# Kernel optimization log

Measured on AMD Instinct MI355X. Metric: run time of the kernel, lower is better.

The kernel has to match this reference:

```python
import jax, jax.numpy as jnp
import numpy as np

EMBED_DIM = 1024
NUM_HEADS = 16
HEAD_DIM = EMBED_DIM // NUM_HEADS


def setup_inputs() -> dict:
    key = jax.random.key(0)
    ks = jax.random.split(key, 5)
    s = 0.02
    return {
        "x": jax.random.normal(ks[0], (2, 2048, EMBED_DIM), dtype=jnp.float32),
        "w_qkv": jax.random.normal(ks[1], (EMBED_DIM, 3 * EMBED_DIM), dtype=jnp.float32) * s,
        "b_qkv": jnp.zeros((3 * EMBED_DIM,), dtype=jnp.float32),
        "w_out": jax.random.normal(ks[2], (EMBED_DIM, EMBED_DIM), dtype=jnp.float32) * s,
        "b_out": jnp.zeros((EMBED_DIM,), dtype=jnp.float32),
    }


def reference(x, w_qkv, b_qkv, w_out, b_out):
    B, T, C = x.shape
    qkv = x @ w_qkv + b_qkv                       # [B,T,3C]
    q, k, v = jnp.split(qkv, 3, axis=-1)
    # [B,T,C] -> [B,H,T,Dh]
    def heads(t):
        return t.reshape(B, T, NUM_HEADS, HEAD_DIM).transpose(0, 2, 1, 3)
    q, k, v = heads(q), heads(k), heads(v)
    scale = 1.0 / np.sqrt(HEAD_DIM).astype(np.float32)
    scores = jnp.einsum("bhqd,bhkd->bhqk", q, k) * scale  # [B,H,T,T]
    causal = jnp.tril(jnp.ones((T, T), dtype=bool))
    scores = jnp.where(causal[None, None], scores, -jnp.inf)
    attn = jax.nn.softmax(scores, axis=-1)
    out = jnp.einsum("bhqk,bhkd->bhqd", attn, v)  # [B,H,T,Dh]
    out = out.transpose(0, 2, 1, 3).reshape(B, T, C)
    return out @ w_out + b_out
```

## Files before the change

kernel.cpp:

```cpp
#include <hip/hip_runtime.h>

typedef unsigned short u16;
typedef unsigned int u32;
typedef __attribute__((ext_vector_type(2))) unsigned int u32x2;
typedef __attribute__((ext_vector_type(8))) short bf16x8;
typedef __attribute__((ext_vector_type(4))) float f32x4;
typedef __attribute__((ext_vector_type(16))) float f32x16;

#define TOK   4096
#define EMB   1024
#define NQKV  3072
#define TSEQ  2048
#define NH    16

__device__ __forceinline__ u16 f2b(float f) {
  union { float f; unsigned u; } v; v.f = f;
  unsigned r = v.u + 0x7FFFu + ((v.u >> 16) & 1u);
  return (u16)(r >> 16);
}

__device__ __forceinline__ u16 f2b_hu(float f) {
  return (u16)((__float_as_uint(f) + 0x8000u) >> 16);
}

__device__ __forceinline__ u32 pack_rn(float a, float b) {
  u32 ua = __float_as_uint(a) + 0x8000u;
  u32 ub = __float_as_uint(b) + 0x8000u;
  return __builtin_amdgcn_perm(ub, ua, 0x07060302u);
}

__device__ __forceinline__ f32x16 zero16() {
  f32x16 z;
#pragma unroll
  for (int i = 0; i < 16; i++) z[i] = 0.f;
  return z;
}

__device__ __forceinline__ void gload16(const void* g, void* l) {
  __builtin_amdgcn_global_load_lds((const __attribute__((address_space(1))) void*)g,
                                   (__attribute__((address_space(3))) void*)l, 16, 0, 0);
}


__global__ __launch_bounds__(256) void prep_kernel(const float* __restrict__ x,
                                                   u16* __restrict__ x_bf,
                                                   const float* __restrict__ w_qkv,
                                                   u16* __restrict__ wqkvT,
                                                   const float* __restrict__ w_out,
                                                   u16* __restrict__ woutT) {
  __shared__ u16 sm[64][65];
  int bid = blockIdx.x, tid = threadIdx.x;
  if (bid < 4096) {
    int i = bid * 256 + tid;
    float4 v = ((const float4*)x)[i];
    union { u16 us[4]; uint2 u2; } o;
    o.us[0] = f2b(v.x); o.us[1] = f2b(v.y); o.us[2] = f2b(v.z); o.us[3] = f2b(v.w);
    ((uint2*)x_bf)[i] = o.u2;
    return;
  }
  const float* src; u16* dst; int R, C, bx, by;
  if (bid < 4096 + 768) {
    int t = bid - 4096; bx = t % 48; by = t / 48;
    src = w_qkv; dst = wqkvT; R = EMB; C = NQKV;
  } else {
    int t = bid - 4096 - 768; bx = t & 15; by = t >> 4;
    src = w_out; dst = woutT; R = EMB; C = EMB;
  }
  int c0 = bx * 64, r0 = by * 64;
#pragma unroll
  for (int i = 0; i < 16; i++) {
    int idx = tid + i * 256;
    int r = idx >> 6, c = idx & 63;
    sm[r][c] = f2b(src[(size_t)(r0 + r) * C + c0 + c]);
  }
  __syncthreads();
  int cc2 = tid >> 2, rr0 = (tid & 3) * 16;
  union { u16 us[16]; uint4 v4[2]; } o;
#pragma unroll
  for (int j = 0; j < 16; j++) o.us[j] = sm[rr0 + j][cc2];
  *(uint4*)&dst[(size_t)(c0 + cc2) * R + r0 + rr0]     = o.v4[0];
  *(uint4*)&dst[(size_t)(c0 + cc2) * R + r0 + rr0 + 8] = o.v4[1];
}


template <int MODE, int TN>
__global__ __launch_bounds__(256) void gemm_bt(const u16* __restrict__ A,
                                               const u16* __restrict__ Bt,
                                               const float* __restrict__ bias,
                                               u16* __restrict__ qb, u16* __restrict__ kb,
                                               u16* __restrict__ vb, float* __restrict__ outp,
                                               int K, int N) {
  constexpr int CT = TN / 32;
  constexpr int RB = TN / 32;
  __shared__ u16 As[2][128][64];
  __shared__ u16 Bs[2][TN][64];
  int tid = threadIdx.x;
  int m0 = blockIdx.y * 128, n0 = blockIdx.x * TN;
  int lane = tid & 63, wid = tid >> 6;
  int wm = (wid >> 1) * 64;
  int wn = (wid & 1) * (TN / 2);
  int l15 = lane & 15, quad = lane >> 4;
  int srow = lane >> 3;
  int scol = (((lane & 7) ^ srow) * 8);

  f32x4 acc[4][CT];
#pragma unroll
  for (int i = 0; i < 4; i++)
#pragma unroll
    for (int j = 0; j < CT; j++) acc[i][j] = (f32x4){0.f, 0.f, 0.f, 0.f};

  const u16* Ag = A + (size_t)(m0 + wid * 32 + srow) * K + scol;
  const u16* Bg = Bt + (size_t)(n0 + wid * (TN / 4) + srow) * K + scol;

#pragma unroll
  for (int i = 0; i < 4; i++)
    gload16(Ag + (size_t)(i * 8) * K, &As[0][wid * 32 + i * 8][0]);
#pragma unroll
  for (int i = 0; i < RB; i++)
    gload16(Bg + (size_t)(i * 8) * K, &Bs[0][wid * (TN / 4) + i * 8][0]);
  __syncthreads();

  int cur = 0;
  for (int k0 = 0; k0 < K; k0 += 64) {
    if (k0 + 64 < K) {
      int kn = k0 + 64;
#pragma unroll
      for (int i = 0; i < 4; i++)
        gload16(Ag + (size_t)(i * 8) * K + kn, &As[cur ^ 1][wid * 32 + i * 8][0]);
#pragma unroll
      for (int i = 0; i < RB; i++)
        gload16(Bg + (size_t)(i * 8) * K + kn, &Bs[cur ^ 1][wid * (TN / 4) + i * 8][0]);
    }

#pragma unroll
    for (int ks = 0; ks < 2; ks++) {
      bf16x8 af[4], bfr[CT];
#pragma unroll
      for (int rt = 0; rt < 4; rt++)
        af[rt] = *(const bf16x8*)&As[cur][wm + rt * 16 + l15][((ks * 4 + quad) ^ (l15 & 7)) * 8];
#pragma unroll
      for (int ct = 0; ct < CT; ct++)
        bfr[ct] = *(const bf16x8*)&Bs[cur][wn + ct * 16 + l15][((ks * 4 + quad) ^ (l15 & 7)) * 8];
#pragma unroll
      for (int rt = 0; rt < 4; rt++)
#pragma unroll
        for (int ct = 0; ct < CT; ct++)
          acc[rt][ct] = __builtin_amdgcn_mfma_f32_16x16x32_bf16(bfr[ct], af[rt], acc[rt][ct], 0, 0, 0);
    }
    __syncthreads();
    cur ^= 1;
  }

#pragma unroll
  for (int rt = 0; rt < 4; rt++) {
#pragma unroll
    for (int ct = 0; ct < CT; ct++) {
      int m = m0 + wm + rt * 16 + l15;
      int nb = n0 + wn + ct * 16 + quad * 4;
      float4 b4 = *(const float4*)&bias[nb];
      float v0 = acc[rt][ct][0] + b4.x, v1 = acc[rt][ct][1] + b4.y;
      float v2 = acc[rt][ct][2] + b4.z, v3 = acc[rt][ct][3] + b4.w;
      if (MODE == 0) {
        int sel = nb >> 10;
        int c = nb & 1023;
        int h = c >> 6, d0 = c & 63;
        int b = m >> 11, t = m & 2047;
        if (sel == 2) {
          size_t vbase = ((((size_t)b * NH + h) * 64 + d0) * TSEQ) + t;
          vb[vbase]            = f2b_hu(v0);
          vb[vbase + TSEQ]     = f2b_hu(v1);
          vb[vbase + 2 * TSEQ] = f2b_hu(v2);
          vb[vbase + 3 * TSEQ] = f2b_hu(v3);
        } else {
          u16* dst = sel ? kb : qb;
          union { u32 u[2]; uint2 u2; } o;
          o.u[0] = pack_rn(v0, v1);
          o.u[1] = pack_rn(v2, v3);
          *(uint2*)&dst[((((size_t)b * NH + h) * TSEQ + t) << 6) + d0] = o.u2;
        }
      } else {
        float4 o = {v0, v1, v2, v3};
        *(float4*)&outp[(size_t)m * N + nb] = o;
      }
    }
  }
}


__global__ __launch_bounds__(256, 4) void attn_kernel(const u16* __restrict__ Qb,
                                                      const u16* __restrict__ Kb,
                                                      const u16* __restrict__ Vtb,
                                                      u16* __restrict__ O) {
  __shared__ u16 Ks[64][68];
  __shared__ u16 Vt[64][68];
  __shared__ float Cmb[2][16][64][2];
  __shared__ float Lmb[2][32];

  const float SCL = 0.18033688f;
  const float MOFF = 16.0f;

  int phys = blockIdx.x;
  int xcd = phys & 7;
  int cuL = (phys >> 3) & 31;
  int slot = phys >> 8;
  int bh = xcd * 4 + slot;
  int qt = (slot & 1) ? (31 - cuL) : cuL;

  int tid = threadIdx.x, lane = tid & 63, w = tid >> 6;
  int sub = w & 1, par = w >> 1;
  int l31 = lane & 31, h = lane >> 5;
  const size_t hoff = (size_t)bh * TSEQ * 64;

  int qw = qt * 64 + sub * 32;
  int qg = qw + l31;

  bf16x8 qf[4];
  {
    const u16* qp = Qb + hoff + (size_t)qg * 64 + h * 8;
#pragma unroll
    for (int s = 0; s < 4; s++) qf[s] = *(const bf16x8*)(qp + s * 16);
  }

  f32x16 acc[2];
  acc[0] = zero16(); acc[1] = zero16();
  float l_i = 0.f;

  int r = tid >> 2, cb = (tid & 3) * 16;
  bf16x8 kr0, kr1, vr0, vr1;
  {
    const u16* kg = Kb + hoff + (size_t)r * 64 + cb;
    const u16* vg = Vtb + hoff + (size_t)r * TSEQ + cb;
    kr0 = *(const bf16x8*)kg;       kr1 = *(const bf16x8*)(kg + 8);
    vr0 = *(const bf16x8*)vg;       vr1 = *(const bf16x8*)(vg + 8);
  }

  for (int kt = 0; kt <= qt; kt++) {
    __syncthreads();
    *(bf16x8*)&Ks[r][cb]     = kr0;
    *(bf16x8*)&Ks[r][cb + 8] = kr1;
    *(bf16x8*)&Vt[r][cb]     = vr0;
    *(bf16x8*)&Vt[r][cb + 8] = vr1;
    __syncthreads();
    if (kt < qt) {
      const u16* kg = Kb + hoff + (size_t)((kt + 1) * 64 + r) * 64 + cb;
      const u16* vg = Vtb + hoff + (size_t)r * TSEQ + (kt + 1) * 64 + cb;
      kr0 = *(const bf16x8*)kg;     kr1 = *(const bf16x8*)(kg + 8);
      vr0 = *(const bf16x8*)vg;     vr1 = *(const bf16x8*)(vg + 8);
    }

    int kbt = kt * 64 + par * 32;
    if (kbt <= qw + 31) {
      f32x16 sacc = zero16();
#pragma unroll
      for (int s = 0; s < 4; s++) {
        bf16x8 kf = *(const bf16x8*)&Ks[par * 32 + l31][s * 16 + h * 8];
        sacc = __builtin_amdgcn_mfma_f32_32x32x16_bf16(kf, qf[s], sacc, 0, 0, 0);
      }

      if (kbt + 31 > qw) {
#pragma unroll
        for (int rr = 0; rr < 16; rr++) {
          int key = kbt + (rr & 3) + 8 * (rr >> 2) + 4 * h;
          if (key > qg) sacc[rr] = -1e30f;
        }
      }

#pragma unroll
      for (int rr = 0; rr < 16; rr++) {
        float p = exp2f(__builtin_fmaf(sacc[rr], SCL, -MOFF));
        sacc[rr] = p;
        l_i += p;
      }

#pragma unroll
      for (int s2 = 0; s2 < 2; s2++) {
        u32 u0, u1, u2, u3;
        asm("v_cvt_pk_bf16_f32 %0, %1, %2" : "=v"(u0) : "v"(sacc[8 * s2 + 0]), "v"(sacc[8 * s2 + 1]));
        asm("v_cvt_pk_bf16_f32 %0, %1, %2" : "=v"(u1) : "v"(sacc[8 * s2 + 2]), "v"(sacc[8 * s2 + 3]));
        asm("v_cvt_pk_bf16_f32 %0, %1, %2" : "=v"(u2) : "v"(sacc[8 * s2 + 4]), "v"(sacc[8 * s2 + 5]));
        asm("v_cvt_pk_bf16_f32 %0, %1, %2" : "=v"(u3) : "v"(sacc[8 * s2 + 6]), "v"(sacc[8 * s2 + 7]));
        u32x2 r02 = __builtin_amdgcn_permlane32_swap(u0, u2, false, false);
        u32x2 r13 = __builtin_amdgcn_permlane32_swap(u1, u3, false, false);
        union { u32 d[4]; bf16x8 v; } pf;
        pf.d[0] = r02[0];
        pf.d[1] = r13[0];
        pf.d[2] = r02[1];
        pf.d[3] = r13[1];
#pragma unroll
        for (int dt = 0; dt < 2; dt++) {
          bf16x8 vf = *(const bf16x8*)&Vt[dt * 32 + l31][par * 32 + s2 * 16 + h * 8];
          acc[dt] = __builtin_amdgcn_mfma_f32_32x32x16_bf16(vf, pf.v, acc[dt], 0, 0, 0);
        }
      }
    }
  }

  l_i += __shfl_xor(l_i, 32);

  __syncthreads();
  if (par == 1) {
#pragma unroll
    for (int dt = 0; dt < 2; dt++)
#pragma unroll
      for (int pr = 0; pr < 8; pr++) {
        Cmb[sub][dt * 8 + pr][lane][0] = acc[dt][2 * pr];
        Cmb[sub][dt * 8 + pr][lane][1] = acc[dt][2 * pr + 1];
      }
    if (h == 0) Lmb[sub][l31] = l_i;
  }
  __syncthreads();
  if (par == 0) {
#pragma unroll
    for (int dt = 0; dt < 2; dt++)
#pragma unroll
      for (int pr = 0; pr < 8; pr++) {
        acc[dt][2 * pr]     += Cmb[sub][dt * 8 + pr][lane][0];
        acc[dt][2 * pr + 1] += Cmb[sub][dt * 8 + pr][lane][1];
      }
    float lt = l_i + Lmb[sub][l31];
    float inv = 1.0f / lt;

    int b = bh >> 4, head = bh & 15;
    size_t rowbase = ((size_t)b * TSEQ + qg) * 1024 + head * 64;
#pragma unroll
    for (int dt = 0; dt < 2; dt++)
#pragma unroll
      for (int G = 0; G < 4; G++) {
        union { u32 u[2]; uint2 u2; } o;
        o.u[0] = pack_rn(acc[dt][4 * G + 0] * inv, acc[dt][4 * G + 1] * inv);
        o.u[1] = pack_rn(acc[dt][4 * G + 2] * inv, acc[dt][4 * G + 3] * inv);
        *(uint2*)&O[rowbase + dt * 32 + G * 8 + 4 * h] = o.u2;
      }
  }
}


extern "C" void kernel_launch(void* const* d_in, const int* in_sizes, int n_in,
                              void* d_out, int out_size, void* d_ws, size_t ws_size,
                              hipStream_t stream) {
  (void)in_sizes; (void)n_in; (void)out_size; (void)ws_size;
  const float* x     = (const float*)d_in[0];
  const float* w_qkv = (const float*)d_in[1];
  const float* b_qkv = (const float*)d_in[2];
  const float* w_out = (const float*)d_in[3];
  const float* b_out = (const float*)d_in[4];
  float* out = (float*)d_out;

  char* p = (char*)d_ws;
  u16* x_bf  = (u16*)p; p += (size_t)TOK * EMB * 2;
  u16* wqkvT = (u16*)p; p += (size_t)NQKV * EMB * 2;
  u16* woutT = (u16*)p; p += (size_t)EMB * EMB * 2;
  u16* Qb    = (u16*)p; p += (size_t)32 * TSEQ * 64 * 2;
  u16* Kb    = (u16*)p; p += (size_t)32 * TSEQ * 64 * 2;
  u16* Vtb   = (u16*)p; p += (size_t)32 * TSEQ * 64 * 2;
  u16* attn_o = (u16*)p;

  prep_kernel<<<dim3(4096 + 768 + 256), 256, 0, stream>>>(x, x_bf, w_qkv, wqkvT, w_out, woutT);
  gemm_bt<0, 128><<<dim3(NQKV / 128, TOK / 128), 256, 0, stream>>>(x_bf, wqkvT, b_qkv,
                                                                   Qb, Kb, Vtb, nullptr, EMB, NQKV);
  attn_kernel<<<dim3(1024), 256, 0, stream>>>(Qb, Kb, Vtb, attn_o);
  gemm_bt<1, 64><<<dim3(EMB / 64, TOK / 128), 256, 0, stream>>>(attn_o, woutT, b_out,
                                                                nullptr, nullptr, nullptr, out, EMB, EMB);
}
```

Measured before the change: 182.9 us.

## Pipeline GEMM K-loop with four-stage LDS ring and explicit vmcnt waits

The GEMM's double-buffered 64-wide K loop becomes a 4-slot ring of 32-wide K tiles. Global-to-LDS loads are issued two steps ahead and each step does a single barrier guarded by explicit s_waitcnt vmcnt, replacing the full __syncthreads per iteration. It also switches to a new rotation-based LDS swizzle, makes K a compile-time constant, and adds a launch_bounds occupancy hint of 2 blocks. The goal is to hide global load latency and cut barrier stalls. The cost is reliance on hand-counted vmcnt values and a specialisation to K=1024.

```diff
diff --git a/kernel.cpp b/kernel.cpp
--- a/kernel.cpp
+++ b/kernel.cpp
@@ -84,24 +84,27 @@
 
 
 template <int MODE, int TN>
-__global__ __launch_bounds__(256) void gemm_bt(const u16* __restrict__ A,
-                                               const u16* __restrict__ Bt,
-                                               const float* __restrict__ bias,
-                                               u16* __restrict__ qb, u16* __restrict__ kb,
-                                               u16* __restrict__ vb, float* __restrict__ outp,
-                                               int K, int N) {
+__global__ __launch_bounds__(256, 2) void gemm_bt(const u16* __restrict__ A,
+                                                  const u16* __restrict__ Bt,
+                                                  const float* __restrict__ bias,
+                                                  u16* __restrict__ qb, u16* __restrict__ kb,
+                                                  u16* __restrict__ vb, float* __restrict__ outp,
+                                                  int N) {
+  constexpr int K = 1024;
+  constexpr int NSTEP = K / 32;
   constexpr int CT = TN / 32;
-  constexpr int RB = TN / 32;
-  __shared__ u16 As[2][128][64];
-  __shared__ u16 Bs[2][TN][64];
+  constexpr int BL = TN / 64;
+  constexpr int LPS = 2 + BL;
+  __shared__ u16 As[4][128][32];
+  __shared__ u16 Bs[4][TN][32];
   int tid = threadIdx.x;
   int m0 = blockIdx.y * 128, n0 = blockIdx.x * TN;
   int lane = tid & 63, wid = tid >> 6;
   int wm = (wid >> 1) * 64;
   int wn = (wid & 1) * (TN / 2);
   int l15 = lane & 15, quad = lane >> 4;
-  int srow = lane >> 3;
-  int scol = (((lane & 7) ^ srow) * 8);
+  int srow = lane >> 2;
+  int sgrp = ((lane & 3) - (lane >> 3)) & 3;
 
   f32x4 acc[4][CT];
 #pragma unroll
@@ -109,47 +112,55 @@
 #pragma unroll
     for (int j = 0; j < CT; j++) acc[i][j] = (f32x4){0.f, 0.f, 0.f, 0.f};
 
-  const u16* Ag = A + (size_t)(m0 + wid * 32 + srow) * K + scol;
-  const u16* Bg = Bt + (size_t)(n0 + wid * (TN / 4) + srow) * K + scol;
-
-#pragma unroll
-  for (int i = 0; i < 4; i++)
-    gload16(Ag + (size_t)(i * 8) * K, &As[0][wid * 32 + i * 8][0]);
-#pragma unroll
-  for (int i = 0; i < RB; i++)
-    gload16(Bg + (size_t)(i * 8) * K, &Bs[0][wid * (TN / 4) + i * 8][0]);
-  __syncthreads();
-
-  int cur = 0;
-  for (int k0 = 0; k0 < K; k0 += 64) {
-    if (k0 + 64 < K) {
-      int kn = k0 + 64;
-#pragma unroll
-      for (int i = 0; i < 4; i++)
-        gload16(Ag + (size_t)(i * 8) * K + kn, &As[cur ^ 1][wid * 32 + i * 8][0]);
-#pragma unroll
-      for (int i = 0; i < RB; i++)
-        gload16(Bg + (size_t)(i * 8) * K + kn, &Bs[cur ^ 1][wid * (TN / 4) + i * 8][0]);
-    }
-
-#pragma unroll
-    for (int ks = 0; ks < 2; ks++) {
-      bf16x8 af[4], bfr[CT];
-#pragma unroll
-      for (int rt = 0; rt < 4; rt++)
-        af[rt] = *(const bf16x8*)&As[cur][wm + rt * 16 + l15][((ks * 4 + quad) ^ (l15 & 7)) * 8];
+  const u16* Ag = A + (size_t)(m0 + wid * 32 + srow) * K + sgrp * 8;
+  const u16* Bg = Bt + (size_t)(n0 + wid * (TN / 4) + srow) * K + sgrp * 8;
+
+  auto stage = [&](int t) {
+#pragma unroll
+    for (int i = 0; i < 2; i++)
+      gload16(Ag + (size_t)(i * 16) * K + t * 32, &As[t & 3][wid * 32 + i * 16][0]);
+#pragma unroll
+    for (int i = 0; i < BL; i++)
+      gload16(Bg + (size_t)(i * 16) * K + t * 32, &Bs[t & 3][wid * (TN / 4) + i * 16][0]);
+  };
+
+  auto compute = [&](int t) {
+    int bb = t & 3;
+    bf16x8 af[4], bfr[CT];
+#pragma unroll
+    for (int rt = 0; rt < 4; rt++) {
+      int r = wm + rt * 16 + l15;
+      af[rt] = *(const bf16x8*)&As[bb][r][((quad + (r >> 1)) & 3) * 8];
+    }
+#pragma unroll
+    for (int ct = 0; ct < CT; ct++) {
+      int r = wn + ct * 16 + l15;
+      bfr[ct] = *(const bf16x8*)&Bs[bb][r][((quad + (r >> 1)) & 3) * 8];
+    }
+#pragma unroll
+    for (int rt = 0; rt < 4; rt++)
 #pragma unroll
       for (int ct = 0; ct < CT; ct++)
-        bfr[ct] = *(const bf16x8*)&Bs[cur][wn + ct * 16 + l15][((ks * 4 + quad) ^ (l15 & 7)) * 8];
-#pragma unroll
-      for (int rt = 0; rt < 4; rt++)
-#pragma unroll
-        for (int ct = 0; ct < CT; ct++)
-          acc[rt][ct] = __builtin_amdgcn_mfma_f32_16x16x32_bf16(bfr[ct], af[rt], acc[rt][ct], 0, 0, 0);
-    }
-    __syncthreads();
-    cur ^= 1;
-  }
+        acc[rt][ct] = __builtin_amdgcn_mfma_f32_16x16x32_bf16(bfr[ct], af[rt], acc[rt][ct], 0, 0, 0);
+  };
+
+  stage(0);
+  stage(1);
+
+  for (int k = 0; k < NSTEP - 2; ++k) {
+    if constexpr (LPS == 4) asm volatile("s_waitcnt vmcnt(4)" ::: "memory");
+    else                    asm volatile("s_waitcnt vmcnt(3)" ::: "memory");
+    __builtin_amdgcn_s_barrier();
+    stage(k + 2);
+    compute(k);
+  }
+  if constexpr (LPS == 4) asm volatile("s_waitcnt vmcnt(4)" ::: "memory");
+  else                    asm volatile("s_waitcnt vmcnt(3)" ::: "memory");
+  __builtin_amdgcn_s_barrier();
+  compute(NSTEP - 2);
+  asm volatile("s_waitcnt vmcnt(0)" ::: "memory");
+  __builtin_amdgcn_s_barrier();
+  compute(NSTEP - 1);
 
 #pragma unroll
   for (int rt = 0; rt < 4; rt++) {
@@ -357,8 +368,8 @@
 
   prep_kernel<<<dim3(4096 + 768 + 256), 256, 0, stream>>>(x, x_bf, w_qkv, wqkvT, w_out, woutT);
   gemm_bt<0, 128><<<dim3(NQKV / 128, TOK / 128), 256, 0, stream>>>(x_bf, wqkvT, b_qkv,
-                                                                   Qb, Kb, Vtb, nullptr, EMB, NQKV);
+                                                                   Qb, Kb, Vtb, nullptr, NQKV);
   attn_kernel<<<dim3(1024), 256, 0, stream>>>(Qb, Kb, Vtb, attn_o);
   gemm_bt<1, 64><<<dim3(EMB / 64, TOK / 128), 256, 0, stream>>>(attn_o, woutT, b_out,
-                                                                nullptr, nullptr, nullptr, out, EMB, EMB);
-}
+                                                                nullptr, nullptr, nullptr, out, EMB);
+}
```

New measurement: 194.3 us. 1.06x slower.

## Enlarge attention query tile to 128 rows and drop split-key combine

Applied to the files above, without the earlier changes.

Each attention block now handles 128 query rows, four waves of 32 rows each, and every wave walks all keys itself. This replaces the earlier scheme where two waves split the keys of a 64-row tile and merged partial accumulators through shared memory. The grid is halved and the block-to-tile mapping is redone to balance the causal work. Each K/V tile loaded into LDS now serves twice as many queries and the combine step with its extra syncs is gone. In exchange there are fewer blocks, a lower occupancy hint, and longer serial loops per wave.

```diff
diff --git a/kernel.cpp b/kernel.cpp
--- a/kernel.cpp
+++ b/kernel.cpp
@@ -187,31 +187,28 @@
 }
 
 
-__global__ __launch_bounds__(256, 4) void attn_kernel(const u16* __restrict__ Qb,
+__global__ __launch_bounds__(256, 2) void attn_kernel(const u16* __restrict__ Qb,
                                                       const u16* __restrict__ Kb,
                                                       const u16* __restrict__ Vtb,
                                                       u16* __restrict__ O) {
   __shared__ u16 Ks[64][68];
   __shared__ u16 Vt[64][68];
-  __shared__ float Cmb[2][16][64][2];
-  __shared__ float Lmb[2][32];
 
   const float SCL = 0.18033688f;
   const float MOFF = 16.0f;
 
   int phys = blockIdx.x;
   int xcd = phys & 7;
-  int cuL = (phys >> 3) & 31;
-  int slot = phys >> 8;
-  int bh = xcd * 4 + slot;
-  int qt = (slot & 1) ? (31 - cuL) : cuL;
-
-  int tid = threadIdx.x, lane = tid & 63, w = tid >> 6;
-  int sub = w & 1, par = w >> 1;
+  int loc = phys >> 3;
+  int bh = xcd * 4 + (loc & 3);
+  int j = loc >> 2;
+  int qt = (j < 8) ? j : (23 - j);
+
+  int tid = threadIdx.x, lane = tid & 63, sub = tid >> 6;
   int l31 = lane & 31, h = lane >> 5;
   const size_t hoff = (size_t)bh * TSEQ * 64;
 
-  int qw = qt * 64 + sub * 32;
+  int qw = qt * 128 + sub * 32;
   int qg = qw + l31;
 
   bf16x8 qf[4];
@@ -234,104 +231,85 @@
     vr0 = *(const bf16x8*)vg;       vr1 = *(const bf16x8*)(vg + 8);
   }
 
-  for (int kt = 0; kt <= qt; kt++) {
+  int ktmax = 2 * qt + 1;
+  for (int kt = 0; kt <= ktmax; kt++) {
     __syncthreads();
     *(bf16x8*)&Ks[r][cb]     = kr0;
     *(bf16x8*)&Ks[r][cb + 8] = kr1;
     *(bf16x8*)&Vt[r][cb]     = vr0;
     *(bf16x8*)&Vt[r][cb + 8] = vr1;
     __syncthreads();
-    if (kt < qt) {
+    if (kt < ktmax) {
       const u16* kg = Kb + hoff + (size_t)((kt + 1) * 64 + r) * 64 + cb;
       const u16* vg = Vtb + hoff + (size_t)r * TSEQ + (kt + 1) * 64 + cb;
       kr0 = *(const bf16x8*)kg;     kr1 = *(const bf16x8*)(kg + 8);
       vr0 = *(const bf16x8*)vg;     vr1 = *(const bf16x8*)(vg + 8);
     }
 
-    int kbt = kt * 64 + par * 32;
-    if (kbt <= qw + 31) {
-      f32x16 sacc = zero16();
-#pragma unroll
-      for (int s = 0; s < 4; s++) {
-        bf16x8 kf = *(const bf16x8*)&Ks[par * 32 + l31][s * 16 + h * 8];
-        sacc = __builtin_amdgcn_mfma_f32_32x32x16_bf16(kf, qf[s], sacc, 0, 0, 0);
+#pragma unroll
+    for (int pc = 0; pc < 2; pc++) {
+      int kbt = kt * 64 + pc * 32;
+      if (kbt <= qw + 31) {
+        f32x16 sacc = zero16();
+#pragma unroll
+        for (int s = 0; s < 4; s++) {
+          bf16x8 kf = *(const bf16x8*)&Ks[pc * 32 + l31][s * 16 + h * 8];
+          sacc = __builtin_amdgcn_mfma_f32_32x32x16_bf16(kf, qf[s], sacc, 0, 0, 0);
+        }
+
+        if (kbt + 31 > qw) {
+#pragma unroll
+          for (int rr = 0; rr < 16; rr++) {
+            int key = kbt + (rr & 3) + 8 * (rr >> 2) + 4 * h;
+            if (key > qg) sacc[rr] = -1e30f;
+          }
+        }
+
+#pragma unroll
+        for (int rr = 0; rr < 16; rr++) {
+          float p = exp2f(__builtin_fmaf(sacc[rr], SCL, -MOFF));
+          sacc[rr] = p;
+          l_i += p;
+        }
+
+#pragma unroll
+        for (int s2 = 0; s2 < 2; s2++) {
+          u32 u0, u1, u2, u3;
+          asm("v_cvt_pk_bf16_f32 %0, %1, %2" : "=v"(u0) : "v"(sacc[8 * s2 + 0]), "v"(sacc[8 * s2 + 1]));
+          asm("v_cvt_pk_bf16_f32 %0, %1, %2" : "=v"(u1) : "v"(sacc[8 * s2 + 2]), "v"(sacc[8 * s2 + 3]));
+          asm("v_cvt_pk_bf16_f32 %0, %1, %2" : "=v"(u2) : "v"(sacc[8 * s2 + 4]), "v"(sacc[8 * s2 + 5]));
+          asm("v_cvt_pk_bf16_f32 %0, %1, %2" : "=v"(u3) : "v"(sacc[8 * s2 + 6]), "v"(sacc[8 * s2 + 7]));
+          u32x2 r02 = __builtin_amdgcn_permlane32_swap(u0, u2, false, false);
+          u32x2 r13 = __builtin_amdgcn_permlane32_swap(u1, u3, false, false);
+          union { u32 d[4]; bf16x8 v; } pf;
+          pf.d[0] = r02[0];
+          pf.d[1] = r13[0];
+          pf.d[2] = r02[1];
+          pf.d[3] = r13[1];
+#pragma unroll
+          for (int dt = 0; dt < 2; dt++) {
+            bf16x8 vf = *(const bf16x8*)&Vt[dt * 32 + l31][pc * 32 + s2 * 16 + h * 8];
+            acc[dt] = __builtin_amdgcn_mfma_f32_32x32x16_bf16(vf, pf.v, acc[dt], 0, 0, 0);
+          }
+        }
       }
-
-      if (kbt + 31 > qw) {
-#pragma unroll
-        for (int rr = 0; rr < 16; rr++) {
-          int key = kbt + (rr & 3) + 8 * (rr >> 2) + 4 * h;
-          if (key > qg) sacc[rr] = -1e30f;
-        }
-      }
-
-#pragma unroll
-      for (int rr = 0; rr < 16; rr++) {
-        float p = exp2f(__builtin_fmaf(sacc[rr], SCL, -MOFF));
-        sacc[rr] = p;
-        l_i += p;
-      }
-
-#pragma unroll
-      for (int s2 = 0; s2 < 2; s2++) {
-        u32 u0, u1, u2, u3;
-        asm("v_cvt_pk_bf16_f32 %0, %1, %2" : "=v"(u0) : "v"(sacc[8 * s2 + 0]), "v"(sacc[8 * s2 + 1]));
-        asm("v_cvt_pk_bf16_f32 %0, %1, %2" : "=v"(u1) : "v"(sacc[8 * s2 + 2]), "v"(sacc[8 * s2 + 3]));
-        asm("v_cvt_pk_bf16_f32 %0, %1, %2" : "=v"(u2) : "v"(sacc[8 * s2 + 4]), "v"(sacc[8 * s2 + 5]));
-        asm("v_cvt_pk_bf16_f32 %0, %1, %2" : "=v"(u3) : "v"(sacc[8 * s2 + 6]), "v"(sacc[8 * s2 + 7]));
-        u32x2 r02 = __builtin_amdgcn_permlane32_swap(u0, u2, false, false);
-        u32x2 r13 = __builtin_amdgcn_permlane32_swap(u1, u3, false, false);
-        union { u32 d[4]; bf16x8 v; } pf;
-        pf.d[0] = r02[0];
-        pf.d[1] = r13[0];
-        pf.d[2] = r02[1];
-        pf.d[3] = r13[1];
-#pragma unroll
-        for (int dt = 0; dt < 2; dt++) {
-          bf16x8 vf = *(const bf16x8*)&Vt[dt * 32 + l31][par * 32 + s2 * 16 + h * 8];
-          acc[dt] = __builtin_amdgcn_mfma_f32_32x32x16_bf16(vf, pf.v, acc[dt], 0, 0, 0);
-        }
-      }
     }
   }
 
   l_i += __shfl_xor(l_i, 32);
-
-  __syncthreads();
-  if (par == 1) {
-#pragma unroll
-    for (int dt = 0; dt < 2; dt++)
-#pragma unroll
-      for (int pr = 0; pr < 8; pr++) {
-        Cmb[sub][dt * 8 + pr][lane][0] = acc[dt][2 * pr];
-        Cmb[sub][dt * 8 + pr][lane][1] = acc[dt][2 * pr + 1];
-      }
-    if (h == 0) Lmb[sub][l31] = l_i;
-  }
-  __syncthreads();
-  if (par == 0) {
-#pragma unroll
-    for (int dt = 0; dt < 2; dt++)
-#pragma unroll
-      for (int pr = 0; pr < 8; pr++) {
-        acc[dt][2 * pr]     += Cmb[sub][dt * 8 + pr][lane][0];
-        acc[dt][2 * pr + 1] += Cmb[sub][dt * 8 + pr][lane][1];
-      }
-    float lt = l_i + Lmb[sub][l31];
-    float inv = 1.0f / lt;
-
-    int b = bh >> 4, head = bh & 15;
-    size_t rowbase = ((size_t)b * TSEQ + qg) * 1024 + head * 64;
-#pragma unroll
-    for (int dt = 0; dt < 2; dt++)
-#pragma unroll
-      for (int G = 0; G < 4; G++) {
-        union { u32 u[2]; uint2 u2; } o;
-        o.u[0] = pack_rn(acc[dt][4 * G + 0] * inv, acc[dt][4 * G + 1] * inv);
-        o.u[1] = pack_rn(acc[dt][4 * G + 2] * inv, acc[dt][4 * G + 3] * inv);
-        *(uint2*)&O[rowbase + dt * 32 + G * 8 + 4 * h] = o.u2;
-      }
-  }
+  float inv = 1.0f / l_i;
+
+  int b = bh >> 4, head = bh & 15;
+  size_t rowbase = ((size_t)b * TSEQ + qg) * 1024 + head * 64;
+#pragma unroll
+  for (int dt = 0; dt < 2; dt++)
+#pragma unroll
+    for (int G = 0; G < 4; G++) {
+      union { u32 u[2]; uint2 u2; } o;
+      o.u[0] = pack_rn(acc[dt][4 * G + 0] * inv, acc[dt][4 * G + 1] * inv);
+      o.u[1] = pack_rn(acc[dt][4 * G + 2] * inv, acc[dt][4 * G + 3] * inv);
+      *(uint2*)&O[rowbase + dt * 32 + G * 8 + 4 * h] = o.u2;
+    }
 }
 
 
@@ -358,7 +336,7 @@
   prep_kernel<<<dim3(4096 + 768 + 256), 256, 0, stream>>>(x, x_bf, w_qkv, wqkvT, w_out, woutT);
   gemm_bt<0, 128><<<dim3(NQKV / 128, TOK / 128), 256, 0, stream>>>(x_bf, wqkvT, b_qkv,
                                                                    Qb, Kb, Vtb, nullptr, EMB, NQKV);
-  attn_kernel<<<dim3(1024), 256, 0, stream>>>(Qb, Kb, Vtb, attn_o);
+  attn_kernel<<<dim3(512), 256, 0, stream>>>(Qb, Kb, Vtb, attn_o);
   gemm_bt<1, 64><<<dim3(EMB / 64, TOK / 128), 256, 0, stream>>>(attn_o, woutT, b_out,
                                                                 nullptr, nullptr, nullptr, out, EMB, EMB);
 }
```

New measurement: 189.0 us. 3.4% more time.
